# Kernel optimization log

Measured on AMD Instinct MI355X. Metric: run time of the kernel, lower is better.

## Reference

```python
import jax, jax.numpy as jnp
import numpy as np

BATCH = 128
SEQ_CTX = 64          # seq_len - 1 context steps
INPUT_SIZE = 320
OUTPUT_SIZE = 64
ITEM_DIM = INPUT_SIZE - OUTPUT_SIZE   # 256
HIDDEN = 1024
ONE_HOT = 192
BETA = 1.0


def setup_inputs() -> dict:
    key = jax.random.key(0)
    ks = jax.random.split(key, 6)
    return {
        "x_c": jax.random.normal(ks[0], (BATCH, SEQ_CTX, INPUT_SIZE), dtype=jnp.float32),
        "x_q": jax.random.normal(ks[1], (BATCH, ITEM_DIM), dtype=jnp.float32),
        "context_input": jax.random.uniform(ks[2], (BATCH, SEQ_CTX, ONE_HOT), dtype=jnp.float32),
        # W_hi initialized uniform(0, 0.5) as in the torch module
        "W_hi": jax.random.uniform(ks[3], (BATCH, HIDDEN, ITEM_DIM), dtype=jnp.float32) * 0.5,
        "W_oh": jax.random.uniform(ks[4], (BATCH, OUTPUT_SIZE, HIDDEN), dtype=jnp.float32),
        "W_reinst": jax.random.uniform(ks[5], (BATCH, HIDDEN, ONE_HOT), dtype=jnp.float32),
    }


def _context_scan(x_c, context_input, W_hi, W_oh, W_reinst):
    """Sequential one-winner Hebbian updates over the context sequence."""
    def step(carry, xs):
        W_hi, W_oh, W_reinst = carry
        x_curr, ctx = xs                              # (B, INPUT_SIZE), (B, ONE_HOT)
        x_item = x_curr[:, :ITEM_DIM]                 # (B, ITEM_DIM)
        x_label = x_curr[:, ITEM_DIM:]                # (B, OUTPUT_SIZE)
        logits = jnp.einsum('bhd,bd->bh', W_hi, x_item)
        # winner-take-all: one-hot of top-1 hidden unit (sparsify_tensor, k=1)
        z = jax.nn.one_hot(jnp.argmax(logits, axis=1), HIDDEN, dtype=W_hi.dtype)
        zc = z[:, :, None]                            # (B, H, 1)
        # W += z (x - W) : winner row overwritten with current pattern
        W_reinst = W_reinst + zc * (ctx[:, None, :] - W_reinst)
        W_hi = W_hi + zc * (x_item[:, None, :] - W_hi)
        W_oh = W_oh + z[:, None, :] * (x_label[:, :, None] - W_oh)
        return (W_hi, W_oh, W_reinst), None

    xs = (jnp.moveaxis(x_c, 1, 0), jnp.moveaxis(context_input, 1, 0))
    (W_hi, W_oh, W_reinst), _ = jax.lax.scan(step, (W_hi, W_oh, W_reinst), xs)
    return W_hi, W_oh, W_reinst


def reference(x_c, x_q, context_input, W_hi, W_oh, W_reinst):
    W_hi, W_oh, W_reinst = _context_scan(x_c, context_input, W_hi, W_oh, W_reinst)
    # query step
    logits = jnp.einsum('bhd,bd->bh', W_hi, x_q)          # (B, H)
    a = jax.nn.softmax(BETA * logits, axis=1)             # (B, H)
    out = jnp.einsum('boh,bh->bo', W_oh, a)               # (B, OUTPUT_SIZE)
    reinst_context = jnp.einsum('bhc,bh->bc', W_reinst, a)  # (B, ONE_HOT)
    return out, reinst_context
```

## Files before the change

### kernel.cpp

```cpp
#include <hip/hip_runtime.h>
#include <math.h>

#define BATCH 128
#define SEQ 64
#define IN 320
#define OUT 64
#define ITEM 256
#define HID 1024
#define OH 192
#define T65 65

__global__ __launch_bounds__(256) void k_gemm(
    const float* __restrict__ W_hi, const float* __restrict__ x_c,
    const float* __restrict__ x_q, float* __restrict__ G, float* __restrict__ X)
{
  const int b = blockIdx.y;
  const int tile = blockIdx.x;
  const int tid = threadIdx.x;
  const int lane = tid & 63;
  const int wv = __builtin_amdgcn_readfirstlane(tid >> 6);
  const bool isW = (tile < 16);

  __shared__ float Ws[64][65];

  const float* rowbase;
  int rstride;
  if (isW) { rowbase = W_hi + ((size_t)b * HID + (size_t)tile * 64) * ITEM; rstride = ITEM; }
  else     { rowbase = x_c + (size_t)b * SEQ * IN;                           rstride = IN; }

  const float* xs = x_c + (size_t)b * SEQ * IN;
  const float* xq = x_q + (size_t)b * ITEM;

  float acc[17];
  #pragma unroll
  for (int i = 0; i < 17; ++i) acc[i] = 0.f;

  const int t0 = wv * 16;

  for (int kc = 0; kc < ITEM; kc += 64) {
    __syncthreads();
    {
      const int r = tid >> 4;
      const int k4 = (tid & 15) << 2;
      #pragma unroll
      for (int p = 0; p < 4; ++p) {
        const int rr = r + (p << 4);
        const float4 w = *reinterpret_cast<const float4*>(rowbase + (size_t)rr * rstride + kc + k4);
        Ws[rr][k4 + 0] = w.x; Ws[rr][k4 + 1] = w.y;
        Ws[rr][k4 + 2] = w.z; Ws[rr][k4 + 3] = w.w;
      }
    }
    __syncthreads();
    #pragma unroll 4
    for (int k = 0; k < 64; k += 4) {
      const float w0 = Ws[lane][k + 0];
      const float w1 = Ws[lane][k + 1];
      const float w2 = Ws[lane][k + 2];
      const float w3 = Ws[lane][k + 3];
      #pragma unroll
      for (int j = 0; j < 16; ++j) {
        const float4 xv = *reinterpret_cast<const float4*>(xs + (size_t)(t0 + j) * IN + kc + k);
        acc[j] = fmaf(w3, xv.w, fmaf(w2, xv.z, fmaf(w1, xv.y, fmaf(w0, xv.x, acc[j]))));
      }
      if (wv == 0) {
        const float4 xv = *reinterpret_cast<const float4*>(xq + kc + k);
        acc[16] = fmaf(w3, xv.w, fmaf(w2, xv.z, fmaf(w1, xv.y, fmaf(w0, xv.x, acc[16]))));
      }
    }
  }

  if (isW) {
    const int h = tile * 64 + lane;
    #pragma unroll
    for (int j = 0; j < 16; ++j)
      G[((size_t)b * T65 + (t0 + j)) * HID + h] = acc[j];
    if (wv == 0)
      G[((size_t)b * T65 + 64) * HID + h] = acc[16];
  } else {
    const int s = lane;
    #pragma unroll
    for (int j = 0; j < 16; ++j)
      X[((size_t)b * T65 + (t0 + j)) * SEQ + s] = acc[j];
    if (wv == 0)
      X[((size_t)b * T65 + 64) * SEQ + s] = acc[16];
  }
}

__global__ __launch_bounds__(256) void k_scan(
    const float* __restrict__ G, const float* __restrict__ X,
    float* __restrict__ a_mod, int* __restrict__ t_s, float* __restrict__ t_a,
    int* __restrict__ t_n)
{
  const int b = blockIdx.x;
  const int tid = threadIdx.x;
  const int lane = tid & 63;
  const int wv = tid >> 6;

  __shared__ float Xs[T65 * SEQ];
  __shared__ int lastw[HID];
  __shared__ float rv[4];
  __shared__ int rh[4];
  __shared__ float redm[4];
  __shared__ float reds[4];
  __shared__ int cnt;

  for (int i = tid; i < T65 * SEQ; i += 256)
    Xs[i] = X[(size_t)b * (T65 * SEQ) + i];
  #pragma unroll
  for (int i = 0; i < 4; ++i) lastw[tid + (i << 8)] = -1;
  if (tid == 0) cnt = 0;
  __syncthreads();

  float gcur[4];
  {
    const float* G0 = G + (size_t)b * T65 * HID;
    #pragma unroll
    for (int i = 0; i < 4; ++i) gcur[i] = G0[tid + (i << 8)];
  }

  for (int t = 0; t < SEQ; ++t) {
    const float* Gn = G + ((size_t)b * T65 + (t + 1)) * HID;
    float gnext[4];
    #pragma unroll
    for (int i = 0; i < 4; ++i) gnext[i] = Gn[tid + (i << 8)];

    float bv = -1e30f; int bh = 0;
    #pragma unroll
    for (int i = 0; i < 4; ++i) {
      const int h = tid + (i << 8);
      const int lw = lastw[h];
      const int idx = lw < 0 ? 0 : lw;
      const float xv = Xs[t * SEQ + idx];
      const float v = (lw < 0) ? gcur[i] : xv;
      if (v > bv || (v == bv && h < bh)) { bv = v; bh = h; }
    }
    #pragma unroll
    for (int m = 1; m < 64; m <<= 1) {
      const float ov = __shfl_xor(bv, m, 64);
      const int oh = __shfl_xor(bh, m, 64);
      if (ov > bv || (ov == bv && oh < bh)) { bv = ov; bh = oh; }
    }
    if (lane == 0) { rv[wv] = bv; rh[wv] = bh; }
    __syncthreads();
    if (tid == 0) {
      float fv = rv[0]; int fh = rh[0];
      #pragma unroll
      for (int w = 1; w < 4; ++w)
        if (rv[w] > fv || (rv[w] == fv && rh[w] < fh)) { fv = rv[w]; fh = rh[w]; }
      lastw[fh] = t;
    }
    __syncthreads();
    #pragma unroll
    for (int i = 0; i < 4; ++i) gcur[i] = gnext[i];
  }

  float l[4]; int lw4[4];
  #pragma unroll
  for (int i = 0; i < 4; ++i) {
    const int h = tid + (i << 8);
    const int lw = lastw[h];
    lw4[i] = lw;
    const int idx = lw < 0 ? 0 : lw;
    l[i] = (lw < 0) ? gcur[i] : Xs[64 * SEQ + idx];
  }
  float mx = fmaxf(fmaxf(l[0], l[1]), fmaxf(l[2], l[3]));
  #pragma unroll
  for (int m = 1; m < 64; m <<= 1) mx = fmaxf(mx, __shfl_xor(mx, m, 64));
  if (lane == 0) redm[wv] = mx;
  __syncthreads();
  const float M = fmaxf(fmaxf(redm[0], redm[1]), fmaxf(redm[2], redm[3]));
  float e[4];
  float ssum = 0.f;
  #pragma unroll
  for (int i = 0; i < 4; ++i) { e[i] = expf(l[i] - M); ssum += e[i]; }
  #pragma unroll
  for (int m = 1; m < 64; m <<= 1) ssum += __shfl_xor(ssum, m, 64);
  if (lane == 0) reds[wv] = ssum;
  __syncthreads();
  const float S = reds[0] + reds[1] + reds[2] + reds[3];
  const float inv = 1.f / S;
  #pragma unroll
  for (int i = 0; i < 4; ++i) {
    const int h = tid + (i << 8);
    const float a = e[i] * inv;
    float am = a;
    if (lw4[i] >= 0) {
      am = 0.f;
      const int slot = atomicAdd(&cnt, 1);
      t_s[b * SEQ + slot] = lw4[i];
      t_a[b * SEQ + slot] = a;
    }
    a_mod[(size_t)b * HID + h] = am;
  }
  __syncthreads();
  if (tid == 0) t_n[b] = cnt;
}

__global__ __launch_bounds__(256) void k_partial(
    const float* __restrict__ W_oh, const float* __restrict__ W_re,
    const float* __restrict__ a_mod, float* __restrict__ p_out, float* __restrict__ p_re)
{
  const int b = blockIdx.y;
  const int p = blockIdx.x;
  const int tid = threadIdx.x;
  const int h0 = p * 256;
  __shared__ float as[256];
  as[tid] = a_mod[(size_t)b * HID + h0 + tid];
  __syncthreads();

  const int wv = tid >> 6, lane = tid & 63;
  if (wv < 3) {
    const int c = tid;
    const float* Wr = W_re + ((size_t)b * HID + h0) * OH + c;
    float acc = 0.f;
    #pragma unroll 8
    for (int h = 0; h < 256; ++h)
      acc = fmaf(Wr[(size_t)h * OH], as[h], acc);
    p_re[((size_t)b * 4 + p) * OH + c] = acc;
  } else {
    for (int o = 0; o < 64; ++o) {
      const float4 w4 = *reinterpret_cast<const float4*>(
          W_oh + ((size_t)b * OUT + o) * HID + h0 + lane * 4);
      const float* ap = &as[lane * 4];
      float acc = w4.x * ap[0] + w4.y * ap[1] + w4.z * ap[2] + w4.w * ap[3];
      #pragma unroll
      for (int m = 1; m < 64; m <<= 1) acc += __shfl_xor(acc, m, 64);
      if (lane == 0) p_out[((size_t)b * 4 + p) * OUT + o] = acc;
    }
  }
}

__global__ __launch_bounds__(256) void k_final(
    const float* __restrict__ x_c, const float* __restrict__ ctx,
    const float* __restrict__ p_out, const float* __restrict__ p_re,
    const int* __restrict__ t_s, const float* __restrict__ t_a,
    const int* __restrict__ t_n, float* __restrict__ out)
{
  const int b = blockIdx.x;
  const int tid = threadIdx.x;
  __shared__ int ss[64];
  __shared__ float sa[64];
  __shared__ int n_s;
  if (tid == 0) n_s = t_n[b];
  if (tid < 64) { ss[tid] = t_s[b * SEQ + tid]; sa[tid] = t_a[b * SEQ + tid]; }
  __syncthreads();
  const int n = n_s;
  if (tid < 64) {
    const int o = tid;
    float acc = 0.f;
    #pragma unroll
    for (int p = 0; p < 4; ++p) acc += p_out[((size_t)b * 4 + p) * OUT + o];
    for (int j = 0; j < n; ++j)
      acc = fmaf(x_c[((size_t)b * SEQ + ss[j]) * IN + ITEM + o], sa[j], acc);
    out[(size_t)b * OUT + o] = acc;
  } else {
    const int c = tid - 64;
    float acc = 0.f;
    #pragma unroll
    for (int p = 0; p < 4; ++p) acc += p_re[((size_t)b * 4 + p) * OH + c];
    for (int j = 0; j < n; ++j)
      acc = fmaf(ctx[((size_t)b * SEQ + ss[j]) * OH + c], sa[j], acc);
    out[(size_t)BATCH * OUT + (size_t)b * OH + c] = acc;
  }
}

extern "C" void kernel_launch(void* const* d_in, const int* in_sizes, int n_in,
                              void* d_out, int out_size, void* d_ws, size_t ws_size,
                              hipStream_t stream)
{
  const float* x_c  = (const float*)d_in[0];
  const float* x_q  = (const float*)d_in[1];
  const float* ctx  = (const float*)d_in[2];
  const float* W_hi = (const float*)d_in[3];
  const float* W_oh = (const float*)d_in[4];
  const float* W_re = (const float*)d_in[5];

  char* ws = (char*)d_ws;
  float* G     = (float*)(ws);
  float* X     = (float*)(ws + 34078720);
  float* a_mod = (float*)(ws + 36208640);
  int*   t_s   = (int*)  (ws + 36732928);
  float* t_a   = (float*)(ws + 36765696);
  int*   t_n   = (int*)  (ws + 36798464);
  float* p_out = (float*)(ws + 36798976);
  float* p_re  = (float*)(ws + 36930048);

  k_gemm<<<dim3(17, BATCH), 256, 0, stream>>>(W_hi, x_c, x_q, G, X);
  k_scan<<<dim3(BATCH), 256, 0, stream>>>(G, X, a_mod, t_s, t_a, t_n);
  k_partial<<<dim3(4, BATCH), 256, 0, stream>>>(W_oh, W_re, a_mod, p_out, p_re);
  k_final<<<dim3(BATCH), 256, 0, stream>>>(x_c, ctx, p_out, p_re, t_s, t_a, t_n, (float*)d_out);
}
```

Measured before the change: 546.5 us.

## Register-tile the logit GEMM and run the winner scan in a single wavefront

```diff
diff --git a/kernel.cpp b/kernel.cpp
--- a/kernel.cpp
+++ b/kernel.cpp
@@ -1,5 +1,6 @@
 #include <hip/hip_runtime.h>
 #include <math.h>
+#include <float.h>
 
 #define BATCH 128
 #define SEQ 64
@@ -9,199 +10,186 @@
 #define HID 1024
 #define OH 192
 #define T65 65
+#define KC 32
+#define LDW 36
+
+__device__ __forceinline__ void bett(float& bv, int& bh, float v, int h) {
+  if (v > bv || (v == bv && h < bh)) { bv = v; bh = h; }
+}
+
+template<int R>
+__device__ __forceinline__ void gemm_body(
+    const float* __restrict__ wbase, int wstride, int wrows,
+    const float* __restrict__ xcb, const float* __restrict__ xqb,
+    float* __restrict__ Ws, float* __restrict__ Xs,
+    int tid, int lane, float (&acc)[R][8], float (&accq)[R])
+{
+  const int rg = lane >> 3, cg = lane & 7;
+  const int wv = tid >> 6;
+  const int rowbase = wv * (8 * R);
+
+  for (int kc = 0; kc < ITEM; kc += KC) {
+    __syncthreads();
+    const int nunit = wrows * (KC / 4);
+    for (int u = tid; u < nunit; u += 256) {
+      const int row = u >> 3, kq = (u & 7) << 2;
+      const float4 v = *reinterpret_cast<const float4*>(wbase + (size_t)row * wstride + kc + kq);
+      *reinterpret_cast<float4*>(&Ws[row * LDW + kq]) = v;
+    }
+    for (int u = tid; u < T65 * (KC / 4); u += 256) {
+      const int row = u >> 3, kq = (u & 7) << 2;
+      const float* src = (row < 64) ? (xcb + (size_t)row * IN) : xqb;
+      const float4 v = *reinterpret_cast<const float4*>(src + kc + kq);
+      *reinterpret_cast<float4*>(&Xs[row * LDW + kq]) = v;
+    }
+    __syncthreads();
+
+    #pragma unroll
+    for (int ks = 0; ks < KC; ks += 4) {
+      float4 wf[R];
+      #pragma unroll
+      for (int i = 0; i < R; ++i)
+        wf[i] = *reinterpret_cast<const float4*>(&Ws[(rowbase + rg + 8 * i) * LDW + ks]);
+      const float4 qf = *reinterpret_cast<const float4*>(&Xs[64 * LDW + ks]);
+      #pragma unroll
+      for (int j = 0; j < 8; ++j) {
+        const float4 xf = *reinterpret_cast<const float4*>(&Xs[(cg + 8 * j) * LDW + ks]);
+        #pragma unroll
+        for (int i = 0; i < R; ++i)
+          acc[i][j] = fmaf(wf[i].w, xf.w, fmaf(wf[i].z, xf.z,
+                      fmaf(wf[i].y, xf.y, fmaf(wf[i].x, xf.x, acc[i][j]))));
+      }
+      #pragma unroll
+      for (int i = 0; i < R; ++i)
+        accq[i] = fmaf(wf[i].w, qf.w, fmaf(wf[i].z, qf.z,
+                  fmaf(wf[i].y, qf.y, fmaf(wf[i].x, qf.x, accq[i]))));
+    }
+  }
+}
 
 __global__ __launch_bounds__(256) void k_gemm(
     const float* __restrict__ W_hi, const float* __restrict__ x_c,
     const float* __restrict__ x_q, float* __restrict__ G, float* __restrict__ X)
 {
-  const int b = blockIdx.y;
-  const int tile = blockIdx.x;
-  const int tid = threadIdx.x;
-  const int lane = tid & 63;
-  const int wv = __builtin_amdgcn_readfirstlane(tid >> 6);
-  const bool isW = (tile < 16);
-
-  __shared__ float Ws[64][65];
-
-  const float* rowbase;
-  int rstride;
-  if (isW) { rowbase = W_hi + ((size_t)b * HID + (size_t)tile * 64) * ITEM; rstride = ITEM; }
-  else     { rowbase = x_c + (size_t)b * SEQ * IN;                           rstride = IN; }
-
-  const float* xs = x_c + (size_t)b * SEQ * IN;
-  const float* xq = x_q + (size_t)b * ITEM;
-
-  float acc[17];
-  #pragma unroll
-  for (int i = 0; i < 17; ++i) acc[i] = 0.f;
-
-  const int t0 = wv * 16;
-
-  for (int kc = 0; kc < ITEM; kc += 64) {
-    __syncthreads();
+  const int b = blockIdx.y, tile = blockIdx.x;
+  const int tid = threadIdx.x, lane = tid & 63;
+  const int rg = lane >> 3, cg = lane & 7, wv = tid >> 6;
+  __shared__ float Ws[256 * LDW];
+  __shared__ float Xs[T65 * LDW];
+  const float* xcb = x_c + (size_t)b * SEQ * IN;
+  const float* xqb = x_q + (size_t)b * ITEM;
+
+  if (tile < 4) {
+    float acc[8][8] = {}; float accq[8] = {};
+    gemm_body<8>(W_hi + ((size_t)b * HID + tile * 256) * ITEM, ITEM, 256,
+                 xcb, xqb, Ws, Xs, tid, lane, acc, accq);
+    const int hb = tile * 256 + wv * 64 + rg;
+    #pragma unroll
+    for (int i = 0; i < 8; ++i) {
+      const int h = hb + 8 * i;
+      #pragma unroll
+      for (int j = 0; j < 8; ++j)
+        G[((size_t)b * T65 + (cg + 8 * j)) * HID + h] = acc[i][j];
+      if (cg == 0) G[((size_t)b * T65 + 64) * HID + h] = accq[i];
+    }
+  } else {
+    float acc[2][8] = {}; float accq[2] = {};
+    gemm_body<2>(xcb, IN, 64, xcb, xqb, Ws, Xs, tid, lane, acc, accq);
+    const int sb = wv * 16 + rg;
+    #pragma unroll
+    for (int i = 0; i < 2; ++i) {
+      const int s = sb + 8 * i;
+      #pragma unroll
+      for (int j = 0; j < 8; ++j)
+        X[((size_t)b * T65 + (cg + 8 * j)) * SEQ + s] = acc[i][j];
+      if (cg == 0) X[((size_t)b * T65 + 64) * SEQ + s] = accq[i];
+    }
+  }
+}
+
+__global__ __launch_bounds__(64) void k_scan(
+    const float* __restrict__ G, const float* __restrict__ X,
+    float* __restrict__ a_mod, float* __restrict__ t_a)
+{
+  const int b = blockIdx.x, lane = threadIdx.x;
+  __shared__ float Xs[T65 * SEQ];
+  {
+    const float4* Xsrc = reinterpret_cast<const float4*>(X + (size_t)b * T65 * SEQ);
+    float4* Xd = reinterpret_cast<float4*>(Xs);
+    for (int i = lane; i < T65 * SEQ / 4; i += 64) Xd[i] = Xsrc[i];
+  }
+  const float* Gb = G + (size_t)b * T65 * HID;
+  float gcur[16];
+  #pragma unroll
+  for (int i = 0; i < 16; ++i) gcur[i] = Gb[lane + 64 * i];
+  __syncthreads();
+
+  unsigned vmask = 0xFFFFu;
+  int myrow = 0x7FFFFFFF;
+  bool active = false;
+
+  for (int t = 0; t < SEQ; ++t) {
+    const float* Gn = Gb + (size_t)(t + 1) * HID;
+    float gnext[16];
+    #pragma unroll
+    for (int i = 0; i < 16; ++i) gnext[i] = Gn[lane + 64 * i];
+
+    float bv = -FLT_MAX; int bh = 0x7FFFFFFF;
+    #pragma unroll
+    for (int i = 0; i < 16; ++i) {
+      const float v = ((vmask >> i) & 1u) ? gcur[i] : -FLT_MAX;
+      bett(bv, bh, v, lane + (i << 6));
+    }
     {
-      const int r = tid >> 4;
-      const int k4 = (tid & 15) << 2;
-      #pragma unroll
-      for (int p = 0; p < 4; ++p) {
-        const int rr = r + (p << 4);
-        const float4 w = *reinterpret_cast<const float4*>(rowbase + (size_t)rr * rstride + kc + k4);
-        Ws[rr][k4 + 0] = w.x; Ws[rr][k4 + 1] = w.y;
-        Ws[rr][k4 + 2] = w.z; Ws[rr][k4 + 3] = w.w;
-      }
-    }
-    __syncthreads();
-    #pragma unroll 4
-    for (int k = 0; k < 64; k += 4) {
-      const float w0 = Ws[lane][k + 0];
-      const float w1 = Ws[lane][k + 1];
-      const float w2 = Ws[lane][k + 2];
-      const float w3 = Ws[lane][k + 3];
-      #pragma unroll
-      for (int j = 0; j < 16; ++j) {
-        const float4 xv = *reinterpret_cast<const float4*>(xs + (size_t)(t0 + j) * IN + kc + k);
-        acc[j] = fmaf(w3, xv.w, fmaf(w2, xv.z, fmaf(w1, xv.y, fmaf(w0, xv.x, acc[j]))));
-      }
-      if (wv == 0) {
-        const float4 xv = *reinterpret_cast<const float4*>(xq + kc + k);
-        acc[16] = fmaf(w3, xv.w, fmaf(w2, xv.z, fmaf(w1, xv.y, fmaf(w0, xv.x, acc[16]))));
-      }
-    }
-  }
-
-  if (isW) {
-    const int h = tile * 64 + lane;
-    #pragma unroll
-    for (int j = 0; j < 16; ++j)
-      G[((size_t)b * T65 + (t0 + j)) * HID + h] = acc[j];
-    if (wv == 0)
-      G[((size_t)b * T65 + 64) * HID + h] = acc[16];
-  } else {
-    const int s = lane;
-    #pragma unroll
-    for (int j = 0; j < 16; ++j)
-      X[((size_t)b * T65 + (t0 + j)) * SEQ + s] = acc[j];
-    if (wv == 0)
-      X[((size_t)b * T65 + 64) * SEQ + s] = acc[16];
-  }
-}
-
-__global__ __launch_bounds__(256) void k_scan(
-    const float* __restrict__ G, const float* __restrict__ X,
-    float* __restrict__ a_mod, int* __restrict__ t_s, float* __restrict__ t_a,
-    int* __restrict__ t_n)
-{
-  const int b = blockIdx.x;
-  const int tid = threadIdx.x;
-  const int lane = tid & 63;
-  const int wv = tid >> 6;
-
-  __shared__ float Xs[T65 * SEQ];
-  __shared__ int lastw[HID];
-  __shared__ float rv[4];
-  __shared__ int rh[4];
-  __shared__ float redm[4];
-  __shared__ float reds[4];
-  __shared__ int cnt;
-
-  for (int i = tid; i < T65 * SEQ; i += 256)
-    Xs[i] = X[(size_t)b * (T65 * SEQ) + i];
-  #pragma unroll
-  for (int i = 0; i < 4; ++i) lastw[tid + (i << 8)] = -1;
-  if (tid == 0) cnt = 0;
-  __syncthreads();
-
-  float gcur[4];
-  {
-    const float* G0 = G + (size_t)b * T65 * HID;
-    #pragma unroll
-    for (int i = 0; i < 4; ++i) gcur[i] = G0[tid + (i << 8)];
-  }
-
-  for (int t = 0; t < SEQ; ++t) {
-    const float* Gn = G + ((size_t)b * T65 + (t + 1)) * HID;
-    float gnext[4];
-    #pragma unroll
-    for (int i = 0; i < 4; ++i) gnext[i] = Gn[tid + (i << 8)];
-
-    float bv = -1e30f; int bh = 0;
-    #pragma unroll
-    for (int i = 0; i < 4; ++i) {
-      const int h = tid + (i << 8);
-      const int lw = lastw[h];
-      const int idx = lw < 0 ? 0 : lw;
-      const float xv = Xs[t * SEQ + idx];
-      const float v = (lw < 0) ? gcur[i] : xv;
-      if (v > bv || (v == bv && h < bh)) { bv = v; bh = h; }
+      const float v = active ? Xs[t * SEQ + lane] : -FLT_MAX;
+      bett(bv, bh, v, myrow);
     }
     #pragma unroll
     for (int m = 1; m < 64; m <<= 1) {
       const float ov = __shfl_xor(bv, m, 64);
       const int oh = __shfl_xor(bh, m, 64);
-      if (ov > bv || (ov == bv && oh < bh)) { bv = ov; bh = oh; }
-    }
-    if (lane == 0) { rv[wv] = bv; rh[wv] = bh; }
-    __syncthreads();
-    if (tid == 0) {
-      float fv = rv[0]; int fh = rh[0];
-      #pragma unroll
-      for (int w = 1; w < 4; ++w)
-        if (rv[w] > fv || (rv[w] == fv && rh[w] < fh)) { fv = rv[w]; fh = rh[w]; }
-      lastw[fh] = t;
-    }
-    __syncthreads();
-    #pragma unroll
-    for (int i = 0; i < 4; ++i) gcur[i] = gnext[i];
-  }
-
-  float l[4]; int lw4[4];
-  #pragma unroll
-  for (int i = 0; i < 4; ++i) {
-    const int h = tid + (i << 8);
-    const int lw = lastw[h];
-    lw4[i] = lw;
-    const int idx = lw < 0 ? 0 : lw;
-    l[i] = (lw < 0) ? gcur[i] : Xs[64 * SEQ + idx];
-  }
-  float mx = fmaxf(fmaxf(l[0], l[1]), fmaxf(l[2], l[3]));
+      bett(bv, bh, ov, oh);
+    }
+    if (active && myrow == bh) active = false;
+    if (lane == t) { active = true; myrow = bh; }
+    if ((bh & 63) == lane) vmask &= ~(1u << (bh >> 6));
+    #pragma unroll
+    for (int i = 0; i < 16; ++i) gcur[i] = gnext[i];
+  }
+
+  float e[16];
+  float mx = -FLT_MAX;
+  #pragma unroll
+  for (int i = 0; i < 16; ++i) {
+    e[i] = ((vmask >> i) & 1u) ? gcur[i] : -FLT_MAX;
+    mx = fmaxf(mx, e[i]);
+  }
+  const float lt = active ? Xs[64 * SEQ + lane] : -FLT_MAX;
+  mx = fmaxf(mx, lt);
   #pragma unroll
   for (int m = 1; m < 64; m <<= 1) mx = fmaxf(mx, __shfl_xor(mx, m, 64));
-  if (lane == 0) redm[wv] = mx;
-  __syncthreads();
-  const float M = fmaxf(fmaxf(redm[0], redm[1]), fmaxf(redm[2], redm[3]));
-  float e[4];
   float ssum = 0.f;
   #pragma unroll
-  for (int i = 0; i < 4; ++i) { e[i] = expf(l[i] - M); ssum += e[i]; }
+  for (int i = 0; i < 16; ++i) {
+    e[i] = ((vmask >> i) & 1u) ? expf(e[i] - mx) : 0.f;
+    ssum += e[i];
+  }
+  const float et = active ? expf(lt - mx) : 0.f;
+  ssum += et;
   #pragma unroll
   for (int m = 1; m < 64; m <<= 1) ssum += __shfl_xor(ssum, m, 64);
-  if (lane == 0) reds[wv] = ssum;
-  __syncthreads();
-  const float S = reds[0] + reds[1] + reds[2] + reds[3];
-  const float inv = 1.f / S;
-  #pragma unroll
-  for (int i = 0; i < 4; ++i) {
-    const int h = tid + (i << 8);
-    const float a = e[i] * inv;
-    float am = a;
-    if (lw4[i] >= 0) {
-      am = 0.f;
-      const int slot = atomicAdd(&cnt, 1);
-      t_s[b * SEQ + slot] = lw4[i];
-      t_a[b * SEQ + slot] = a;
-    }
-    a_mod[(size_t)b * HID + h] = am;
-  }
-  __syncthreads();
-  if (tid == 0) t_n[b] = cnt;
+  const float inv = 1.f / ssum;
+  #pragma unroll
+  for (int i = 0; i < 16; ++i)
+    a_mod[(size_t)b * HID + lane + 64 * i] = e[i] * inv;
+  t_a[b * SEQ + lane] = et * inv;
 }
 
 __global__ __launch_bounds__(256) void k_partial(
     const float* __restrict__ W_oh, const float* __restrict__ W_re,
     const float* __restrict__ a_mod, float* __restrict__ p_out, float* __restrict__ p_re)
 {
-  const int b = blockIdx.y;
-  const int p = blockIdx.x;
+  const int b = blockIdx.y, p = blockIdx.x;
   const int tid = threadIdx.x;
   const int h0 = p * 256;
   __shared__ float as[256];
@@ -233,33 +221,31 @@
 __global__ __launch_bounds__(256) void k_final(
     const float* __restrict__ x_c, const float* __restrict__ ctx,
     const float* __restrict__ p_out, const float* __restrict__ p_re,
-    const int* __restrict__ t_s, const float* __restrict__ t_a,
-    const int* __restrict__ t_n, float* __restrict__ out)
-{
-  const int b = blockIdx.x;
-  const int tid = threadIdx.x;
-  __shared__ int ss[64];
-  __shared__ float sa[64];
-  __shared__ int n_s;
-  if (tid == 0) n_s = t_n[b];
-  if (tid < 64) { ss[tid] = t_s[b * SEQ + tid]; sa[tid] = t_a[b * SEQ + tid]; }
+    const float* __restrict__ t_a, float* __restrict__ out)
+{
+  const int b = blockIdx.x, tid = threadIdx.x;
+  __shared__ float sa[SEQ];
+  if (tid < SEQ) sa[tid] = t_a[b * SEQ + tid];
   __syncthreads();
-  const int n = n_s;
-  if (tid < 64) {
+  if (tid < OUT) {
     const int o = tid;
     float acc = 0.f;
     #pragma unroll
     for (int p = 0; p < 4; ++p) acc += p_out[((size_t)b * 4 + p) * OUT + o];
-    for (int j = 0; j < n; ++j)
-      acc = fmaf(x_c[((size_t)b * SEQ + ss[j]) * IN + ITEM + o], sa[j], acc);
+    for (int j = 0; j < SEQ; ++j) {
+      const float w = sa[j];
+      if (w != 0.f) acc = fmaf(x_c[((size_t)b * SEQ + j) * IN + ITEM + o], w, acc);
+    }
     out[(size_t)b * OUT + o] = acc;
-  } else {
-    const int c = tid - 64;
+  } else if (tid < OUT + OH) {
+    const int c = tid - OUT;
     float acc = 0.f;
     #pragma unroll
     for (int p = 0; p < 4; ++p) acc += p_re[((size_t)b * 4 + p) * OH + c];
-    for (int j = 0; j < n; ++j)
-      acc = fmaf(ctx[((size_t)b * SEQ + ss[j]) * OH + c], sa[j], acc);
+    for (int j = 0; j < SEQ; ++j) {
+      const float w = sa[j];
+      if (w != 0.f) acc = fmaf(ctx[((size_t)b * SEQ + j) * OH + c], w, acc);
+    }
     out[(size_t)BATCH * OUT + (size_t)b * OH + c] = acc;
   }
 }
@@ -279,14 +265,12 @@
   float* G     = (float*)(ws);
   float* X     = (float*)(ws + 34078720);
   float* a_mod = (float*)(ws + 36208640);
-  int*   t_s   = (int*)  (ws + 36732928);
-  float* t_a   = (float*)(ws + 36765696);
-  int*   t_n   = (int*)  (ws + 36798464);
-  float* p_out = (float*)(ws + 36798976);
-  float* p_re  = (float*)(ws + 36930048);
-
-  k_gemm<<<dim3(17, BATCH), 256, 0, stream>>>(W_hi, x_c, x_q, G, X);
-  k_scan<<<dim3(BATCH), 256, 0, stream>>>(G, X, a_mod, t_s, t_a, t_n);
+  float* t_a   = (float*)(ws + 36732928);
+  float* p_out = (float*)(ws + 36765696);
+  float* p_re  = (float*)(ws + 36896768);
+
+  k_gemm<<<dim3(5, BATCH), 256, 0, stream>>>(W_hi, x_c, x_q, G, X);
+  k_scan<<<dim3(BATCH), 64, 0, stream>>>(G, X, a_mod, t_a);
   k_partial<<<dim3(4, BATCH), 256, 0, stream>>>(W_oh, W_re, a_mod, p_out, p_re);
-  k_final<<<dim3(BATCH), 256, 0, stream>>>(x_c, ctx, p_out, p_re, t_s, t_a, t_n, (float*)d_out);
-}
+  k_final<<<dim3(BATCH), 256, 0, stream>>>(x_c, ctx, p_out, p_re, t_a, (float*)d_out);
+}
```

Result: slower. 591.9 us (+8.3%).
